# Performance work log

Measured on AMD Instinct MI355X. Metric: run time of the kernel, lower is better.

## Reference

```python
import jax, jax.numpy as jnp
import numpy as np

NUM_HEADS = 16


def setup_inputs() -> dict:
    key = jax.random.key(0)
    ks = jax.random.split(key, 5)
    B, S, D = 4, 2048, 1024
    scale = 1.0 / np.sqrt(D)
    return {
        "x": jax.random.normal(ks[0], (B, S, D), dtype=jnp.float32),
        "q_proj": jax.random.normal(ks[1], (D, D), dtype=jnp.float32) * scale,
        "k_proj": jax.random.normal(ks[2], (D, D), dtype=jnp.float32) * scale,
        "v_proj": jax.random.normal(ks[3], (D, D), dtype=jnp.float32) * scale,
        "o_proj": jax.random.normal(ks[4], (D, D), dtype=jnp.float32) * scale,
    }


def reference(x, q_proj, k_proj, v_proj, o_proj):
    B, S, D = x.shape
    H = NUM_HEADS
    hd = D // H
    # projections: weight is [d_out, d_in]
    q = jnp.einsum('bsd,kd->bsk', x, q_proj)
    k = jnp.einsum('bsd,kd->bsk', x, k_proj)
    v = jnp.einsum('bsd,kd->bsk', x, v_proj)
    # split heads: [B, H, S, hd]
    q = q.reshape(B, S, H, hd).transpose(0, 2, 1, 3)
    k = k.reshape(B, S, H, hd).transpose(0, 2, 1, 3)
    v = v.reshape(B, S, H, hd).transpose(0, 2, 1, 3)
    scores = jnp.einsum('bhqd,bhkd->bhqk', q, k) / jnp.sqrt(jnp.asarray(hd, dtype=x.dtype))
    causal = jnp.tril(jnp.ones((S, S), dtype=bool))  # True = keep
    scores = jnp.where(causal, scores, -jnp.inf)
    attn = jax.nn.softmax(scores, axis=-1)
    out = jnp.einsum('bhqk,bhkd->bhqd', attn, v)
    out = out.transpose(0, 2, 1, 3).reshape(B, S, D)
    return jnp.einsum('bsv,mv->bsm', out, o_proj)
```

## Files before the change

### kernel.cpp

```cpp
#include <hip/hip_runtime.h>
#include <hip/hip_bf16.h>
#include <stdint.h>


typedef __bf16 bf16x8 __attribute__((ext_vector_type(8)));
typedef __bf16 bf16x4 __attribute__((ext_vector_type(4)));
typedef float  f32x4  __attribute__((ext_vector_type(4)));

static __device__ __forceinline__ f32x4 mfma16(bf16x8 a, bf16x8 b, f32x4 c) {
  return __builtin_amdgcn_mfma_f32_16x16x32_bf16(a, b, c, 0, 0, 0);
}

static __device__ __forceinline__ void load16_lds(const void* g, void* l) {
  __builtin_amdgcn_global_load_lds(
      (const __attribute__((address_space(1))) unsigned int*)g,
      (__attribute__((address_space(3))) unsigned int*)l, 16, 0, 0);
}

__global__ __launch_bounds__(256) void cvt_f32_bf16(
    const float* __restrict__ in, __bf16* __restrict__ out, int n8) {
  int i = blockIdx.x * blockDim.x + threadIdx.x;
  if (i >= n8) return;
  const float4* in4 = (const float4*)in;
  float4 a = in4[2 * i], b = in4[2 * i + 1];
  __bf16 v[8];
  v[0] = (__bf16)a.x; v[1] = (__bf16)a.y; v[2] = (__bf16)a.z; v[3] = (__bf16)a.w;
  v[4] = (__bf16)b.x; v[5] = (__bf16)b.y; v[6] = (__bf16)b.z; v[7] = (__bf16)b.w;
  *(bf16x8*)(out + 8 * i) = *(bf16x8*)v;
}

__global__ __launch_bounds__(256) void cvt_w(
    const float* __restrict__ w0, const float* __restrict__ w1,
    const float* __restrict__ w2, const float* __restrict__ w3,
    __bf16* __restrict__ wqkv, __bf16* __restrict__ wo) {
  int blk = blockIdx.x;
  int m = blk >> 9;
  const float* src = (m == 0) ? w0 : (m == 1) ? w1 : (m == 2) ? w2 : w3;
  __bf16* dst = (m < 3) ? (wqkv + (size_t)m * (1024 * 1024)) : wo;
  const float scl = (m == 0) ? 0.18033688011112042f : 1.0f;
  int i = (blk & 511) * 256 + threadIdx.x;
  const float4* in4 = (const float4*)src;
  float4 a = in4[2 * i], b = in4[2 * i + 1];
  __bf16 v[8];
  v[0] = (__bf16)(a.x * scl); v[1] = (__bf16)(a.y * scl);
  v[2] = (__bf16)(a.z * scl); v[3] = (__bf16)(a.w * scl);
  v[4] = (__bf16)(b.x * scl); v[5] = (__bf16)(b.y * scl);
  v[6] = (__bf16)(b.z * scl); v[7] = (__bf16)(b.w * scl);
  *(bf16x8*)(dst + 8 * i) = *(bf16x8*)v;
}

template <typename OutT>
__global__ __launch_bounds__(256) void gemm_bt2(
    const __bf16* __restrict__ A, const __bf16* __restrict__ Bw,
    OutT* __restrict__ C, int M, int N, int K) {
  __shared__ __align__(16) __bf16 As[128 * 32];
  __shared__ __align__(16) __bf16 Bs[128 * 32];
  const int t = threadIdx.x;
  const int lane = t & 63, w = t >> 6;
  const int wm = w >> 1, wn = w & 1;
  const int l15 = lane & 15, quad = lane >> 4;
  const long rowA0 = (long)blockIdx.y * 128;
  const long rowB0 = (long)blockIdx.x * 128;

  const int r0 = w * 32 + (lane >> 2);
  const int r1 = r0 + 16;
  const int c0 = (lane & 3) ^ ((r0 >> 1) & 3);
  const int c1 = (lane & 3) ^ ((r1 >> 1) & 3);
  const __bf16* pA0 = A + (rowA0 + r0) * (long)K + c0 * 8;
  const __bf16* pA1 = A + (rowA0 + r1) * (long)K + c1 * 8;
  const __bf16* pB0 = Bw + (rowB0 + r0) * (long)K + c0 * 8;
  const __bf16* pB1 = Bw + (rowB0 + r1) * (long)K + c1 * 8;
  __bf16* lA0 = As + (w * 32) * 32;
  __bf16* lA1 = As + (w * 32 + 16) * 32;
  __bf16* lB0 = Bs + (w * 32) * 32;
  __bf16* lB1 = Bs + (w * 32 + 16) * 32;

  int aoff[4], boff[4];
#pragma unroll
  for (int i = 0; i < 4; i++) {
    int Ra = wm * 64 + i * 16 + l15;
    aoff[i] = Ra * 32 + ((quad ^ ((Ra >> 1) & 3)) << 3);
    int Rb = wn * 64 + i * 16 + l15;
    boff[i] = Rb * 32 + ((quad ^ ((Rb >> 1) & 3)) << 3);
  }

  f32x4 acc[4][4] = {};
  for (int k0 = 0; k0 < K; k0 += 32) {
    load16_lds(pA0, lA0); load16_lds(pA1, lA1);
    load16_lds(pB0, lB0); load16_lds(pB1, lB1);
    pA0 += 32; pA1 += 32; pB0 += 32; pB1 += 32;
    __syncthreads();
    bf16x8 af[4], bfr[4];
#pragma unroll
    for (int i = 0; i < 4; i++) af[i] = *(const bf16x8*)(As + aoff[i]);
#pragma unroll
    for (int i = 0; i < 4; i++) bfr[i] = *(const bf16x8*)(Bs + boff[i]);
#pragma unroll
    for (int mt = 0; mt < 4; mt++)
#pragma unroll
      for (int nt = 0; nt < 4; nt++)
        acc[mt][nt] = mfma16(af[mt], bfr[nt], acc[mt][nt]);
    __syncthreads();
  }

#pragma unroll
  for (int mt = 0; mt < 4; mt++)
#pragma unroll
    for (int nt = 0; nt < 4; nt++)
#pragma unroll
      for (int r = 0; r < 4; r++) {
        long row = rowA0 + wm * 64 + mt * 16 + quad * 4 + r;
        long col = rowB0 + wn * 64 + nt * 16 + l15;
        float v = acc[mt][nt][r];
        if constexpr (sizeof(OutT) == 2) C[row * N + col] = (OutT)(__bf16)v;
        else                             C[row * N + col] = v;
      }
}

__global__ __launch_bounds__(256) void vtrans(
    const __bf16* __restrict__ QKV, __bf16* __restrict__ VT) {
  constexpr int LDs = 136;
  __shared__ __align__(16) __bf16 Ts[64 * LDs];
  const int t = threadIdx.x;
  const int st0 = blockIdx.x * 128, h = blockIdx.y, b = blockIdx.z;
  const long vbase = (long)b * 2048 * 3072 + 2048 + h * 64;
#pragma unroll
  for (int i = 0; i < 4; i++) {
    int sl = i * 32 + (t >> 3), d0 = (t & 7) * 8;
    __bf16 tmp[8];
    *(uint4*)tmp = *(const uint4*)(QKV + vbase + (long)(st0 + sl) * 3072 + d0);
#pragma unroll
    for (int j = 0; j < 8; j++) Ts[(d0 + j) * LDs + sl] = tmp[j];
  }
  __syncthreads();
  const long obase = (long)(b * 16 + h) * 64 * 2048 + st0;
  const int d = t >> 2;
#pragma unroll
  for (int i = 0; i < 4; i++) {
    int sc = ((t & 3) + 4 * i) * 8;
    *(uint4*)(VT + obase + (long)d * 2048 + sc) = *(const uint4*)(Ts + d * LDs + sc);
  }
}

__global__ __launch_bounds__(256) void attn4(
    const __bf16* __restrict__ QKV, const __bf16* __restrict__ VT,
    __bf16* __restrict__ O) {
  constexpr int SD = 3072;
  constexpr int LDP = 72;
  __shared__ __align__(16) __bf16 Ks[2][64 * 64];
  __shared__ __align__(16) __bf16 Vs[2][64 * 64];
  __shared__ __align__(16) __bf16 Pw[4 * 32 * LDP];
  const int t = threadIdx.x;
  const int lane = t & 63, w = t >> 6;
  const int l15 = lane & 15, quad = lane >> 4;
  const int jj = blockIdx.x, h = blockIdx.y, b = blockIdx.z;
  const long qbase = (long)b * 2048 * SD + h * 64;
  const long kbase = qbase + 1024;
  const long vtbase = (long)(b * 16 + h) * 64 * 2048;
  __bf16* Pme = Pw + w * 32 * LDP;

  const int sr = w * 16 + (lane >> 3);
  const int scg = (lane & 7) ^ (sr & 7);
  const int ldsOff = (w * 16) * 64;
  const __bf16* gK = QKV + kbase + (long)sr * SD + scg * 8;
  const __bf16* gV = VT + vtbase + (long)sr * 2048 + scg * 8;

  int kvoff[4][2];
#pragma unroll
  for (int nt = 0; nt < 4; nt++)
#pragma unroll
    for (int kk = 0; kk < 2; kk++)
      kvoff[nt][kk] = (nt * 16 + l15) * 64 + (((kk * 4 + quad) ^ (l15 & 7)) << 3);

  bf16x8 ones;
#pragma unroll
  for (int j = 0; j < 8; j++) ones[j] = (__bf16)1.0f;

#pragma unroll
  for (int half = 0; half < 2; half++) {
    const int qt = half ? (15 - jj) : jj;
    const int q0 = qt * 128;
    const int wrow0 = q0 + w * 32;

    bf16x8 qf[2][2];
#pragma unroll
    for (int mt = 0; mt < 2; mt++)
#pragma unroll
      for (int kk = 0; kk < 2; kk++)
        qf[mt][kk] = *(const bf16x8*)(QKV + qbase +
            (long)(wrow0 + mt * 16 + l15) * SD + kk * 32 + quad * 8);

    f32x4 o_acc[2][4] = {};
    f32x4 o_l[2] = {};

    const int nkt = 2 * qt + 2;

    __syncthreads();
    load16_lds(gK, Ks[0] + ldsOff);
    load16_lds(gK + 8 * SD, Ks[0] + ldsOff + 8 * 64);
    load16_lds(gV, Vs[0] + ldsOff);
    load16_lds(gV + 8 * 2048, Vs[0] + ldsOff + 8 * 64);

    int cur = 0;
    for (int kt = 0; kt < nkt; kt++) {
      __syncthreads();
      if (kt + 1 < nkt) {
        const __bf16* gKn = gK + (long)(kt + 1) * 64 * SD;
        const __bf16* gVn = gV + (kt + 1) * 64;
        __bf16* lk = Ks[cur ^ 1] + ldsOff;
        __bf16* lv = Vs[cur ^ 1] + ldsOff;
        load16_lds(gKn, lk);
        load16_lds(gKn + 8 * SD, lk + 8 * 64);
        load16_lds(gVn, lv);
        load16_lds(gVn + 8 * 2048, lv + 8 * 64);
      }

      const int k0 = kt * 64;
      if (k0 <= wrow0 + 31) {
        const __bf16* KsB = Ks[cur];
        const __bf16* VsB = Vs[cur];
        bf16x8 kf[4][2];
#pragma unroll
        for (int nt = 0; nt < 4; nt++)
#pragma unroll
          for (int kk = 0; kk < 2; kk++)
            kf[nt][kk] = *(const bf16x8*)(KsB + kvoff[nt][kk]);
        f32x4 st[4][2];
        __builtin_amdgcn_s_setprio(1);
#pragma unroll
        for (int nt = 0; nt < 4; nt++)
#pragma unroll
          for (int mt = 0; mt < 2; mt++) {
            f32x4 z = {0.f, 0.f, 0.f, 0.f};
            z = mfma16(kf[nt][0], qf[mt][0], z);
            st[nt][mt] = mfma16(kf[nt][1], qf[mt][1], z);
          }
        __builtin_amdgcn_s_setprio(0);

        if (k0 + 63 <= wrow0) {
#pragma unroll
          for (int mt = 0; mt < 2; mt++)
#pragma unroll
            for (int nt = 0; nt < 4; nt++) {
              bf16x4 pb;
#pragma unroll
              for (int r = 0; r < 4; r++)
                pb[r] = (__bf16)__builtin_amdgcn_exp2f(st[nt][mt][r]);
              *(bf16x4*)(Pme + (mt * 16 + l15) * LDP + nt * 16 + quad * 4) = pb;
            }
        } else {
#pragma unroll
          for (int mt = 0; mt < 2; mt++) {
            const int qrow = wrow0 + mt * 16 + l15;
#pragma unroll
            for (int nt = 0; nt < 4; nt++) {
              const int keyb = k0 + nt * 16 + quad * 4;
              bf16x4 pb;
#pragma unroll
              for (int r = 0; r < 4; r++) {
                float e = __builtin_amdgcn_exp2f(st[nt][mt][r]);
                if (keyb + r > qrow) e = 0.f;
                pb[r] = (__bf16)e;
              }
              *(bf16x4*)(Pme + (mt * 16 + l15) * LDP + nt * 16 + quad * 4) = pb;
            }
          }
        }

#pragma unroll
        for (int kk = 0; kk < 2; kk++) {
          bf16x8 vf[4];
#pragma unroll
          for (int dt = 0; dt < 4; dt++)
            vf[dt] = *(const bf16x8*)(VsB + kvoff[dt][kk]);
#pragma unroll
          for (int mt = 0; mt < 2; mt++) {
            bf16x8 pf = *(const bf16x8*)(Pme + (mt * 16 + l15) * LDP + kk * 32 + quad * 8);
            __builtin_amdgcn_s_setprio(1);
#pragma unroll
            for (int dt = 0; dt < 4; dt++)
              o_acc[mt][dt] = mfma16(pf, vf[dt], o_acc[mt][dt]);
            o_l[mt] = mfma16(pf, ones, o_l[mt]);
            __builtin_amdgcn_s_setprio(0);
          }
        }
      }
      cur ^= 1;
    }

#pragma unroll
    for (int mt = 0; mt < 2; mt++) {
#pragma unroll
      for (int r = 0; r < 4; r++) {
        float inv = 1.f / o_l[mt][r];
        int row = wrow0 + mt * 16 + quad * 4 + r;
        long ob = ((long)b * 2048 + row) * 1024 + h * 64;
#pragma unroll
        for (int dt = 0; dt < 4; dt++)
          O[ob + dt * 16 + l15] = (__bf16)(o_acc[mt][dt][r] * inv);
      }
    }
  }
}

extern "C" void kernel_launch(void* const* d_in, const int* in_sizes, int n_in,
                              void* d_out, int out_size, void* d_ws, size_t ws_size,
                              hipStream_t stream) {
  const float* x  = (const float*)d_in[0];
  const float* wq = (const float*)d_in[1];
  const float* wk = (const float*)d_in[2];
  const float* wv = (const float*)d_in[3];
  const float* wo = (const float*)d_in[4];
  float* out = (float*)d_out;

  char* ws = (char*)d_ws;
  __bf16* xb   = (__bf16*)(ws);
  __bf16* wqkv = (__bf16*)(ws + (16l << 20));
  __bf16* wob  = (__bf16*)(ws + (22l << 20));
  __bf16* QKV  = (__bf16*)(ws + (24l << 20));
  __bf16* VT   = (__bf16*)(ws + (72l << 20));
  __bf16* Ab   = xb;

  cvt_f32_bf16<<<4096, 256, 0, stream>>>(x, xb, 8192 * 1024 / 8);
  cvt_w<<<2048, 256, 0, stream>>>(wq, wk, wv, wo, wqkv, wob);

  gemm_bt2<__bf16><<<dim3(24, 64), 256, 0, stream>>>(xb, wqkv, QKV, 8192, 3072, 1024);

  vtrans<<<dim3(16, 16, 4), 256, 0, stream>>>(QKV, VT);

  attn4<<<dim3(8, 16, 4), 256, 0, stream>>>(QKV, VT, Ab);

  gemm_bt2<float><<<dim3(8, 64), 256, 0, stream>>>(Ab, wob, out, 8192, 1024, 1024);
}
```

Baseline: 266.1 us.

## Replace projection GEMMs with 256x256 double-buffered pipelined kernel

Replaces the 128x128, K=32, single-buffered GEMM with a 512-thread 256x256 tile kernel that uses K=64 steps and double-buffered LDS. It interleaves global-to-LDS prefetch of the next tile with MFMA phases, using explicit waitcnt, barriers and setprio. It also adds block-index swizzling for L2 locality. The goal is to hide memory latency and raise arithmetic intensity in both projection GEMMs. The cost is heavy LDS use (128KB) and a small grid, only 128 blocks for the output GEMM, which may underfill the GPU.

Result: slower. 294.0 us (+10.5%).

```diff
diff --git a/kernel.cpp b/kernel.cpp
--- a/kernel.cpp
+++ b/kernel.cpp
@@ -49,71 +49,171 @@
   *(bf16x8*)(dst + 8 * i) = *(bf16x8*)v;
 }
 
+static __device__ __forceinline__ void stage_half(
+    const __bf16* __restrict__ X, long row0, int K, long k0,
+    __bf16* lds, int w, int lane) {
+#pragma unroll
+  for (int j = 0; j < 2; j++) {
+    int rl = j * 64 + w * 8 + (lane >> 3);
+    int chunk = (lane & 7) ^ (rl & 7);
+    load16_lds(X + (row0 + rl) * (long)K + k0 + chunk * 8,
+               lds + (j * 64 + w * 8) * 64);
+  }
+}
+
 template <typename OutT>
-__global__ __launch_bounds__(256) void gemm_bt2(
+__global__ __launch_bounds__(512, 2) void gemm_bt8(
     const __bf16* __restrict__ A, const __bf16* __restrict__ Bw,
-    OutT* __restrict__ C, int M, int N, int K) {
-  __shared__ __align__(16) __bf16 As[128 * 32];
-  __shared__ __align__(16) __bf16 Bs[128 * 32];
+    OutT* __restrict__ C, int M, int N, int K, int NX) {
+  __shared__ __align__(16) __bf16 As[2][256 * 64];
+  __shared__ __align__(16) __bf16 Bs[2][256 * 64];
   const int t = threadIdx.x;
   const int lane = t & 63, w = t >> 6;
-  const int wm = w >> 1, wn = w & 1;
+  const int wm = w >> 2, wn = w & 3;
   const int l15 = lane & 15, quad = lane >> 4;
-  const long rowA0 = (long)blockIdx.y * 128;
-  const long rowB0 = (long)blockIdx.x * 128;
-
-  const int r0 = w * 32 + (lane >> 2);
-  const int r1 = r0 + 16;
-  const int c0 = (lane & 3) ^ ((r0 >> 1) & 3);
-  const int c1 = (lane & 3) ^ ((r1 >> 1) & 3);
-  const __bf16* pA0 = A + (rowA0 + r0) * (long)K + c0 * 8;
-  const __bf16* pA1 = A + (rowA0 + r1) * (long)K + c1 * 8;
-  const __bf16* pB0 = Bw + (rowB0 + r0) * (long)K + c0 * 8;
-  const __bf16* pB1 = Bw + (rowB0 + r1) * (long)K + c1 * 8;
-  __bf16* lA0 = As + (w * 32) * 32;
-  __bf16* lA1 = As + (w * 32 + 16) * 32;
-  __bf16* lB0 = Bs + (w * 32) * 32;
-  __bf16* lB1 = Bs + (w * 32 + 16) * 32;
-
-  int aoff[4], boff[4];
-#pragma unroll
-  for (int i = 0; i < 4; i++) {
-    int Ra = wm * 64 + i * 16 + l15;
-    aoff[i] = Ra * 32 + ((quad ^ ((Ra >> 1) & 3)) << 3);
-    int Rb = wn * 64 + i * 16 + l15;
-    boff[i] = Rb * 32 + ((quad ^ ((Rb >> 1) & 3)) << 3);
+
+  const int bid = blockIdx.x;
+  const int cpx = gridDim.x >> 3;
+  const int swz = (bid & 7) * cpx + (bid >> 3);
+  const long m0 = (long)(swz / NX) * 256;
+  const long n0 = (long)(swz % NX) * 256;
+
+  int aoff[8][2], boff[4][2];
+#pragma unroll
+  for (int mf = 0; mf < 8; mf++)
+#pragma unroll
+    for (int ks = 0; ks < 2; ks++)
+      aoff[mf][ks] = (wm * 128 + mf * 16 + l15) * 64 + (((ks * 4 + quad) ^ (l15 & 7)) << 3);
+#pragma unroll
+  for (int nf = 0; nf < 4; nf++)
+#pragma unroll
+    for (int ks = 0; ks < 2; ks++)
+      boff[nf][ks] = (wn * 64 + nf * 16 + l15) * 64 + (((ks * 4 + quad) ^ (l15 & 7)) << 3);
+
+  const int NT = K >> 6;
+  stage_half(A,  m0,       K, 0,  &As[0][0],        w, lane);
+  stage_half(A,  m0 + 128, K, 0,  &As[0][128 * 64], w, lane);
+  stage_half(Bw, n0,       K, 0,  &Bs[0][0],        w, lane);
+  stage_half(Bw, n0 + 128, K, 0,  &Bs[0][128 * 64], w, lane);
+  stage_half(Bw, n0,       K, 64, &Bs[1][0],        w, lane);
+  asm volatile("s_waitcnt vmcnt(2)" ::: "memory");
+  __builtin_amdgcn_s_barrier();
+
+  f32x4 acc[8][4] = {};
+  for (int T = 0; T < NT; T++) {
+    __bf16* Acur = &As[T & 1][0];
+    __bf16* Bcur = &Bs[T & 1][0];
+    __bf16* Anx  = &As[(T + 1) & 1][0];
+    __bf16* Bnx  = &Bs[(T + 1) & 1][0];
+    const long kn = (long)(T + 1) * 64;
+    const bool pf  = (T + 1 < NT);
+    const bool pf2 = (T + 2 < NT);
+
+    bf16x8 bfr[4][2];
+
+    if (pf) stage_half(A, m0, K, kn, Anx, w, lane);
+#pragma unroll
+    for (int nf = 0; nf < 4; nf++)
+#pragma unroll
+      for (int ks = 0; ks < 2; ks++)
+        bfr[nf][ks] = *(const bf16x8*)(Bcur + boff[nf][ks]);
+    {
+      bf16x8 a00 = *(const bf16x8*)(Acur + aoff[0][0]);
+      bf16x8 a01 = *(const bf16x8*)(Acur + aoff[0][1]);
+      bf16x8 a10 = *(const bf16x8*)(Acur + aoff[1][0]);
+      bf16x8 a11 = *(const bf16x8*)(Acur + aoff[1][1]);
+      __builtin_amdgcn_s_barrier();
+      asm volatile("s_waitcnt lgkmcnt(0)" ::: "memory");
+      __builtin_amdgcn_sched_barrier(0);
+      __builtin_amdgcn_s_setprio(1);
+#pragma unroll
+      for (int nf = 0; nf < 4; nf++) {
+        acc[0][nf] = mfma16(a00, bfr[nf][0], acc[0][nf]);
+        acc[0][nf] = mfma16(a01, bfr[nf][1], acc[0][nf]);
+        acc[1][nf] = mfma16(a10, bfr[nf][0], acc[1][nf]);
+        acc[1][nf] = mfma16(a11, bfr[nf][1], acc[1][nf]);
+      }
+      __builtin_amdgcn_s_setprio(0);
+      __builtin_amdgcn_s_barrier();
+    }
+    if (pf) stage_half(A, m0 + 128, K, kn, Anx + 128 * 64, w, lane);
+    {
+      bf16x8 a00 = *(const bf16x8*)(Acur + aoff[2][0]);
+      bf16x8 a01 = *(const bf16x8*)(Acur + aoff[2][1]);
+      bf16x8 a10 = *(const bf16x8*)(Acur + aoff[3][0]);
+      bf16x8 a11 = *(const bf16x8*)(Acur + aoff[3][1]);
+      __builtin_amdgcn_s_barrier();
+      asm volatile("s_waitcnt lgkmcnt(0)" ::: "memory");
+      __builtin_amdgcn_sched_barrier(0);
+      __builtin_amdgcn_s_setprio(1);
+#pragma unroll
+      for (int nf = 0; nf < 4; nf++) {
+        acc[2][nf] = mfma16(a00, bfr[nf][0], acc[2][nf]);
+        acc[2][nf] = mfma16(a01, bfr[nf][1], acc[2][nf]);
+        acc[3][nf] = mfma16(a10, bfr[nf][0], acc[3][nf]);
+        acc[3][nf] = mfma16(a11, bfr[nf][1], acc[3][nf]);
+      }
+      __builtin_amdgcn_s_setprio(0);
+      __builtin_amdgcn_s_barrier();
+    }
+    if (pf) stage_half(Bw, n0 + 128, K, kn, Bnx + 128 * 64, w, lane);
+    {
+      bf16x8 a00 = *(const bf16x8*)(Acur + aoff[4][0]);
+      bf16x8 a01 = *(const bf16x8*)(Acur + aoff[4][1]);
+      bf16x8 a10 = *(const bf16x8*)(Acur + aoff[5][0]);
+      bf16x8 a11 = *(const bf16x8*)(Acur + aoff[5][1]);
+      __builtin_amdgcn_s_barrier();
+      asm volatile("s_waitcnt lgkmcnt(0)" ::: "memory");
+      __builtin_amdgcn_sched_barrier(0);
+      __builtin_amdgcn_s_setprio(1);
+#pragma unroll
+      for (int nf = 0; nf < 4; nf++) {
+        acc[4][nf] = mfma16(a00, bfr[nf][0], acc[4][nf]);
+        acc[4][nf] = mfma16(a01, bfr[nf][1], acc[4][nf]);
+        acc[5][nf] = mfma16(a10, bfr[nf][0], acc[5][nf]);
+        acc[5][nf] = mfma16(a11, bfr[nf][1], acc[5][nf]);
+      }
+      __builtin_amdgcn_s_setprio(0);
+      __builtin_amdgcn_s_barrier();
+    }
+    {
+      bf16x8 a00 = *(const bf16x8*)(Acur + aoff[6][0]);
+      bf16x8 a01 = *(const bf16x8*)(Acur + aoff[6][1]);
+      bf16x8 a10 = *(const bf16x8*)(Acur + aoff[7][0]);
+      bf16x8 a11 = *(const bf16x8*)(Acur + aoff[7][1]);
+      if (pf2) {
+        stage_half(Bw, n0, K, kn + 64, Bcur, w, lane);
+        asm volatile("s_waitcnt vmcnt(2)" ::: "memory");
+      } else {
+        asm volatile("s_waitcnt vmcnt(0)" ::: "memory");
+      }
+      __builtin_amdgcn_s_barrier();
+      asm volatile("s_waitcnt lgkmcnt(0)" ::: "memory");
+      __builtin_amdgcn_sched_barrier(0);
+      __builtin_amdgcn_s_setprio(1);
+#pragma unroll
+      for (int nf = 0; nf < 4; nf++) {
+        acc[6][nf] = mfma16(a00, bfr[nf][0], acc[6][nf]);
+        acc[6][nf] = mfma16(a01, bfr[nf][1], acc[6][nf]);
+        acc[7][nf] = mfma16(a10, bfr[nf][0], acc[7][nf]);
+        acc[7][nf] = mfma16(a11, bfr[nf][1], acc[7][nf]);
+      }
+      __builtin_amdgcn_s_setprio(0);
+      __builtin_amdgcn_s_barrier();
+    }
   }
 
-  f32x4 acc[4][4] = {};
-  for (int k0 = 0; k0 < K; k0 += 32) {
-    load16_lds(pA0, lA0); load16_lds(pA1, lA1);
-    load16_lds(pB0, lB0); load16_lds(pB1, lB1);
-    pA0 += 32; pA1 += 32; pB0 += 32; pB1 += 32;
-    __syncthreads();
-    bf16x8 af[4], bfr[4];
-#pragma unroll
-    for (int i = 0; i < 4; i++) af[i] = *(const bf16x8*)(As + aoff[i]);
-#pragma unroll
-    for (int i = 0; i < 4; i++) bfr[i] = *(const bf16x8*)(Bs + boff[i]);
-#pragma unroll
-    for (int mt = 0; mt < 4; mt++)
-#pragma unroll
-      for (int nt = 0; nt < 4; nt++)
-        acc[mt][nt] = mfma16(af[mt], bfr[nt], acc[mt][nt]);
-    __syncthreads();
-  }
-
-#pragma unroll
-  for (int mt = 0; mt < 4; mt++)
-#pragma unroll
-    for (int nt = 0; nt < 4; nt++)
+#pragma unroll
+  for (int mf = 0; mf < 8; mf++)
+#pragma unroll
+    for (int nf = 0; nf < 4; nf++)
 #pragma unroll
       for (int r = 0; r < 4; r++) {
-        long row = rowA0 + wm * 64 + mt * 16 + quad * 4 + r;
-        long col = rowB0 + wn * 64 + nt * 16 + l15;
-        float v = acc[mt][nt][r];
-        if constexpr (sizeof(OutT) == 2) C[row * N + col] = (OutT)(__bf16)v;
-        else                             C[row * N + col] = v;
+        long row = m0 + wm * 128 + mf * 16 + quad * 4 + r;
+        long col = n0 + wn * 64 + nf * 16 + l15;
+        float v = acc[mf][nf][r];
+        if constexpr (sizeof(OutT) == 2) C[row * (long)N + col] = (OutT)(__bf16)v;
+        else                             C[row * (long)N + col] = v;
       }
 }
 
@@ -324,11 +424,11 @@
   cvt_f32_bf16<<<4096, 256, 0, stream>>>(x, xb, 8192 * 1024 / 8);
   cvt_w<<<2048, 256, 0, stream>>>(wq, wk, wv, wo, wqkv, wob);
 
-  gemm_bt2<__bf16><<<dim3(24, 64), 256, 0, stream>>>(xb, wqkv, QKV, 8192, 3072, 1024);
+  gemm_bt8<__bf16><<<384, 512, 0, stream>>>(xb, wqkv, QKV, 8192, 3072, 1024, 12);
 
   vtrans<<<dim3(16, 16, 4), 256, 0, stream>>>(QKV, VT);
 
   attn4<<<dim3(8, 16, 4), 256, 0, stream>>>(QKV, VT, Ab);
 
-  gemm_bt2<float><<<dim3(8, 64), 256, 0, stream>>>(Ab, wob, out, 8192, 1024, 1024);
-}
+  gemm_bt8<float><<<128, 512, 0, stream>>>(Ab, wob, out, 8192, 1024, 1024, 4);
+}
```
